# Kernel tuning notes

Measured on AMD Instinct MI355X. Metric: run time of the kernel, lower is better.

Reference implementation:

```python
import jax, jax.numpy as jnp
import numpy as np

N_HEADS = 32
N_KV = 8
HEAD_DIM = 128
THETA = 1000000.0


def setup_inputs() -> dict:
    key = jax.random.key(0)
    ks = jax.random.split(key, 7)
    batch, q_len, history = 4, 1024, 1024
    T = batch * q_len
    H = N_HEADS * HEAD_DIM  # 4096
    kv_len = q_len + history
    block_size = 64
    num_blocks = batch * (kv_len // block_size)  # 128
    s = 0.02
    return {
        'hidden_states': jax.random.normal(ks[0], (T, H), jnp.float32),
        'wq': jax.random.normal(ks[1], (H, N_HEADS * HEAD_DIM), jnp.float32) * s,
        'wk': jax.random.normal(ks[2], (H, N_KV * HEAD_DIM), jnp.float32) * s,
        'wv': jax.random.normal(ks[3], (H, N_KV * HEAD_DIM), jnp.float32) * s,
        'wo': jax.random.normal(ks[4], (N_HEADS * HEAD_DIM, H), jnp.float32) * s,
        'k_cache': jax.random.normal(ks[5], (num_blocks, block_size, N_KV, HEAD_DIM), jnp.float32),
        'v_cache': jax.random.normal(ks[6], (num_blocks, block_size, N_KV, HEAD_DIM), jnp.float32),
        'q_len': q_len,
        'history': history,
        'window': 1024,
    }


def _rotate_half(x):
    d = x.shape[-1]
    return jnp.concatenate([-x[..., d // 2:], x[..., :d // 2]], axis=-1)


def reference(hidden_states, wq, wk, wv, wo, k_cache, v_cache, q_len, history, window):
    T, H = hidden_states.shape
    batch = T // q_len
    kv_len = q_len + history
    nb, bs, n_kv, d = k_cache.shape
    blocks_per_seq = kv_len // bs
    # block table: sequence b owns contiguous blocks (paged layout)
    block_offsets = jnp.arange(batch * blocks_per_seq).reshape(batch, blocks_per_seq)

    # QKV projections
    q = (hidden_states @ wq).reshape(T, N_HEADS, d)
    k = (hidden_states @ wk).reshape(T, n_kv, d)
    v = (hidden_states @ wv).reshape(T, n_kv, d)

    # RoPE using 1d position ids (global positions of new tokens)
    pos = jnp.broadcast_to(history + jnp.arange(q_len), (batch, q_len)).reshape(T)
    inv_freq = 1.0 / (THETA ** (jnp.arange(0, d, 2, dtype=jnp.float32) / d))
    freqs = pos[:, None].astype(jnp.float32) * inv_freq[None, :]
    emb = jnp.concatenate([freqs, freqs], axis=-1)  # [T, d]
    cos = jnp.cos(emb)[:, None, :].astype(q.dtype)
    sin = jnp.sin(emb)[:, None, :].astype(q.dtype)
    q = q * cos + _rotate_half(q) * sin
    k = k * cos + _rotate_half(k) * sin

    # fill_kv_cache: scatter new K/V into paged slots history..kv_len-1
    new_pos = history + jnp.arange(q_len)  # [q_len]
    slot = (block_offsets[:, new_pos // bs] * bs + new_pos % bs).reshape(T)
    k_flat = k_cache.reshape(nb * bs, n_kv, d).at[slot].set(k)
    v_flat = v_cache.reshape(nb * bs, n_kv, d).at[slot].set(v)

    # paged gather of the full KV window per sequence
    all_pos = jnp.arange(kv_len)
    gslot = block_offsets[:, all_pos // bs] * bs + all_pos % bs  # [batch, kv_len]
    k_all = k_flat[gslot]  # [batch, kv_len, n_kv, d]
    v_all = v_flat[gslot]

    # GQA: expand kv heads
    rep = N_HEADS // n_kv
    k_all = jnp.repeat(k_all, rep, axis=2)
    v_all = jnp.repeat(v_all, rep, axis=2)

    qb = q.reshape(batch, q_len, N_HEADS, d)
    scores = jnp.einsum('bqhd,bkhd->bhqk', qb, k_all) / jnp.sqrt(jnp.asarray(d, qb.dtype))

    # causal + sliding-window mask on global positions
    qpos = history + jnp.arange(q_len)
    kpos = jnp.arange(kv_len)
    mask = kpos[None, :] <= qpos[:, None]
    if window > 0:
        mask = mask & ((qpos[:, None] - kpos[None, :]) < window)
    neg = jnp.finfo(scores.dtype).min
    scores = jnp.where(mask[None, None], scores, neg)
    attn = jax.nn.softmax(scores, axis=-1)
    out = jnp.einsum('bhqk,bkhd->bqhd', attn, v_all).reshape(T, N_HEADS * d)
    return out @ wo
```

## Files before the change

### kernel.cpp

```cpp
#include <hip/hip_runtime.h>
#include <hip/hip_bf16.h>

typedef __bf16 bf16x8 __attribute__((ext_vector_type(8)));
typedef __bf16 bf16x4 __attribute__((ext_vector_type(4)));
typedef float  f32x4  __attribute__((ext_vector_type(4)));

#define QL 1024
#define NH 32
#define NKV 8
#define HD 128
#define KVLEN 2048
#define QKV_LD 6144

typedef const __attribute__((address_space(1))) void gv_t;
typedef __attribute__((address_space(3))) void lv_t;
__device__ __forceinline__ void gll16(const void* g, void* l) {
  __builtin_amdgcn_global_load_lds((gv_t*)g, (lv_t*)l, 16, 0, 0);
}

__global__ __launch_bounds__(256) void cast_plain(const float* __restrict__ in,
                                                  __bf16* __restrict__ out, int n4) {
  int i = blockIdx.x * 256 + threadIdx.x;
  if (i >= n4) return;
  float4 v = ((const float4*)in)[i];
  bf16x4 o;
  o[0] = (__bf16)v.x; o[1] = (__bf16)v.y; o[2] = (__bf16)v.z; o[3] = (__bf16)v.w;
  ((bf16x4*)out)[i] = o;
}

__global__ __launch_bounds__(256) void transpose_cast(const float* __restrict__ in,
                                                      __bf16* __restrict__ out,
                                                      int R, int C) {
  __shared__ __bf16 tile[64][65];
  int r0 = blockIdx.y * 64, c0 = blockIdx.x * 64;
  int t = threadIdx.x;
  int tr = t >> 4, tc = (t & 15) * 4;
#pragma unroll
  for (int pass = 0; pass < 4; pass++) {
    int r = pass * 16 + tr;
    float4 v = *(const float4*)(in + (size_t)(r0 + r) * C + c0 + tc);
    tile[r][tc + 0] = (__bf16)v.x;
    tile[r][tc + 1] = (__bf16)v.y;
    tile[r][tc + 2] = (__bf16)v.z;
    tile[r][tc + 3] = (__bf16)v.w;
  }
  __syncthreads();
#pragma unroll
  for (int pass = 0; pass < 4; pass++) {
    int cc = pass * 16 + tr;
    bf16x4 o;
#pragma unroll
    for (int j = 0; j < 4; j++) o[j] = tile[tc + j][cc];
    *(bf16x4*)(out + (size_t)(c0 + cc) * R + r0 + tc) = o;
  }
}

template <int OUT_BF16>
__global__ __launch_bounds__(256) void gemm_bt(const __bf16* __restrict__ A,
                                               const __bf16* __restrict__ Bt,
                                               void* __restrict__ Cout,
                                               int M, int N, int K) {
  __shared__ __attribute__((aligned(16))) __bf16 sA[128 * 32];
  __shared__ __attribute__((aligned(16))) __bf16 sB[128 * 32];
  const int tid = threadIdx.x;
  const int lane = tid & 63;
  const int wave = tid >> 6;
  const int wm = wave >> 1, wn = wave & 1;
  const int quad = lane >> 4, l16 = lane & 15;
  const int row0 = blockIdx.y * 128, col0 = blockIdx.x * 128;

  const int rloc = tid >> 2;
  const int qsel = (tid & 3) ^ ((tid >> 3) & 3);
  const __bf16* gA0 = A + (size_t)(row0 + rloc) * K + qsel * 8;
  const __bf16* gA1 = A + (size_t)(row0 + 64 + rloc) * K + qsel * 8;
  const __bf16* gB0 = Bt + (size_t)(col0 + rloc) * K + qsel * 8;
  const __bf16* gB1 = Bt + (size_t)(col0 + 64 + rloc) * K + qsel * 8;
  __bf16* lA0 = sA + tid * 8;
  __bf16* lA1 = sA + 2048 + tid * 8;
  __bf16* lB0 = sB + tid * 8;
  __bf16* lB1 = sB + 2048 + tid * 8;

  const int xsw = (l16 >> 1) & 3;

  f32x4 acc[4][4];
#pragma unroll
  for (int mt = 0; mt < 4; mt++)
#pragma unroll
    for (int nt = 0; nt < 4; nt++) acc[mt][nt] = (f32x4){0.f, 0.f, 0.f, 0.f};

  for (int k0 = 0; k0 < K; k0 += 32) {
    __syncthreads();
    gll16(gA0 + k0, lA0);
    gll16(gA1 + k0, lA1);
    gll16(gB0 + k0, lB0);
    gll16(gB1 + k0, lB1);
    __syncthreads();
    bf16x8 af[4], bfr[4];
#pragma unroll
    for (int mt = 0; mt < 4; mt++)
      af[mt] = *(const bf16x8*)(sA + (wm * 64 + mt * 16 + l16) * 32 + (quad ^ xsw) * 8);
#pragma unroll
    for (int nt = 0; nt < 4; nt++)
      bfr[nt] = *(const bf16x8*)(sB + (wn * 64 + nt * 16 + l16) * 32 + (quad ^ xsw) * 8);
#pragma unroll
    for (int mt = 0; mt < 4; mt++)
#pragma unroll
      for (int nt = 0; nt < 4; nt++)
        acc[mt][nt] = __builtin_amdgcn_mfma_f32_16x16x32_bf16(af[mt], bfr[nt],
                                                              acc[mt][nt], 0, 0, 0);
  }

#pragma unroll
  for (int mt = 0; mt < 4; mt++) {
#pragma unroll
    for (int r = 0; r < 4; r++) {
      int grow = row0 + wm * 64 + mt * 16 + quad * 4 + r;
#pragma unroll
      for (int nt = 0; nt < 4; nt++) {
        int gcol = col0 + wn * 64 + nt * 16 + l16;
        float v = acc[mt][nt][r];
        if (OUT_BF16)
          ((__bf16*)Cout)[(size_t)grow * N + gcol] = (__bf16)v;
        else
          ((float*)Cout)[(size_t)grow * N + gcol] = v;
      }
    }
  }
}

__global__ __launch_bounds__(256) void rope_kernel(__bf16* __restrict__ qkv) {
  int idx = blockIdx.x * 256 + threadIdx.x;
  int m = idx & 63;
  int rest = idx >> 6;
  int t = rest / 40;
  int head = rest - t * 40;
  int i = t & (QL - 1);
  float pos = (float)(1024 + i);
  float ang = pos * exp2f(-(float)m * 0.31143075889569403f);
  float c = cosf(ang), sn = sinf(ang);
  size_t base = (size_t)t * QKV_LD + head * HD;
  float x0 = (float)qkv[base + m];
  float x1 = (float)qkv[base + 64 + m];
  qkv[base + m]      = (__bf16)(x0 * c - x1 * sn);
  qkv[base + 64 + m] = (__bf16)(x1 * c + x0 * sn);
}

__global__ __launch_bounds__(256) void kv_build_k(const float* __restrict__ kcache,
                                                  const __bf16* __restrict__ qkv,
                                                  __bf16* __restrict__ k_all) {
  int idx = blockIdx.x * 256 + threadIdx.x;
  int d8 = (idx & 15) * 8;
  int p = (idx >> 4) & (KVLEN - 1);
  int bk = idx >> 15;
  int b = bk >> 3, kvh = bk & 7;
  __bf16* dst = k_all + ((size_t)bk * KVLEN + p) * HD + d8;
  if (p < 1024) {
    const float* src = kcache + ((size_t)(b * KVLEN + p) * NKV + kvh) * HD + d8;
    bf16x8 o;
#pragma unroll
    for (int j = 0; j < 8; j++) o[j] = (__bf16)src[j];
    *(bf16x8*)dst = o;
  } else {
    const __bf16* src = qkv + (size_t)(b * QL + p - 1024) * QKV_LD + 4096 + kvh * HD + d8;
    *(bf16x8*)dst = *(const bf16x8*)src;
  }
}

__global__ __launch_bounds__(256) void kv_build_vT(const float* __restrict__ vcache,
                                                   const __bf16* __restrict__ qkv,
                                                   __bf16* __restrict__ v_allT) {
  __shared__ __bf16 tile[64][130];
  int blk = blockIdx.x;
  int pt = blk & 31, bk = blk >> 5;
  int b = bk >> 3, kvh = bk & 7;
  int p0 = pt * 64;
  int t = threadIdx.x;
  int lr = t >> 4, d8 = (t & 15) * 8;
#pragma unroll
  for (int pass = 0; pass < 4; pass++) {
    int pl = pass * 16 + lr;
    int p = p0 + pl;
    if (p < 1024) {
      const float* src = vcache + ((size_t)(b * KVLEN + p) * NKV + kvh) * HD + d8;
#pragma unroll
      for (int j = 0; j < 8; j++) tile[pl][d8 + j] = (__bf16)src[j];
    } else {
      const __bf16* src = qkv + (size_t)(b * QL + p - 1024) * QKV_LD + 5120 + kvh * HD + d8;
      bf16x8 v = *(const bf16x8*)src;
#pragma unroll
      for (int j = 0; j < 8; j++) tile[pl][d8 + j] = v[j];
    }
  }
  __syncthreads();
#pragma unroll
  for (int pass = 0; pass < 4; pass++) {
    int d = (t >> 3) + pass * 32;
    int ps = (t & 7) * 8;
    bf16x8 o;
#pragma unroll
    for (int j = 0; j < 8; j++) o[j] = tile[ps + j][d];
    *(bf16x8*)(v_allT + ((size_t)bk * HD + d) * KVLEN + p0 + ps) = o;
  }
}

__global__ __launch_bounds__(256) void attn_kernel(const __bf16* __restrict__ qkv,
                                                   const __bf16* __restrict__ k_all,
                                                   const __bf16* __restrict__ v_allT,
                                                   __bf16* __restrict__ out) {
  __shared__ __attribute__((aligned(16))) __bf16 sK[64 * 128];
  __shared__ __attribute__((aligned(16))) __bf16 sV[128 * 64];
  __shared__ __attribute__((aligned(16))) __bf16 sP[4][32 * 72];
  const int tid = threadIdx.x;
  const int lane = tid & 63;
  const int wave = tid >> 6;
  const int quad = lane >> 4, l16 = lane & 15;
  const int bid = blockIdx.x;
  const int b = bid & 3;
  const int kvh = (bid >> 2) & 7;
  const int qt = bid >> 5;
  const int h = kvh * 4 + wave;
  const int i0 = qt * 32;

  const __bf16* kb = k_all + (size_t)(b * NKV + kvh) * KVLEN * HD;
  const __bf16* vb = v_allT + (size_t)(b * NKV + kvh) * HD * KVLEN;

  bf16x8 qf[2][4];
#pragma unroll
  for (int mt = 0; mt < 2; mt++) {
    const __bf16* qb = qkv + (size_t)(b * QL + i0 + mt * 16 + l16) * QKV_LD + h * HD + quad * 8;
#pragma unroll
    for (int kc = 0; kc < 4; kc++) qf[mt][kc] = *(const bf16x8*)(qb + kc * 32);
  }

  int kgo[4], vgo[4];
#pragma unroll
  for (int j = 0; j < 4; j++) {
    int g = wave * 4 + j;
    kgo[j] = (g * 4 + quad) * HD + (l16 ^ (g & 7)) * 8;
    int d = g * 8 + (lane >> 3);
    vgo[j] = d * KVLEN + ((lane & 7) ^ ((lane >> 3) & 7)) * 8;
  }
  __bf16* kls = sK + (wave * 4) * 512 + lane * 8;
  __bf16* vls = sV + (wave * 4) * 512 + lane * 8;

  f32x4 o[8][2];
#pragma unroll
  for (int dt = 0; dt < 8; dt++)
#pragma unroll
    for (int mt = 0; mt < 2; mt++) o[dt][mt] = (f32x4){0.f, 0.f, 0.f, 0.f};
  f32x4 lac[2];
  lac[0] = (f32x4){0.f, 0.f, 0.f, 0.f};
  lac[1] = (f32x4){0.f, 0.f, 0.f, 0.f};

  bf16x8 ones;
#pragma unroll
  for (int j = 0; j < 8; j++) ones[j] = (__bf16)1.0f;

  __bf16* myP = &sP[wave][0];
  const float ES = 0.12751744f;

  const int cs = (i0 + 1) & ~63;
  const int xsw = l16 & 7;

#pragma unroll
  for (int j = 0; j < 4; j++) gll16(kb + (size_t)cs * HD + kgo[j], kls + j * 512);
#pragma unroll
  for (int j = 0; j < 4; j++) gll16(vb + (size_t)cs + vgo[j], vls + j * 512);

  for (int ci = 0; ci < 17; ci++) {
    const int c = cs + ci * 64;
    __syncthreads();
    f32x4 s[2][4];
#pragma unroll
    for (int nt = 0; nt < 4; nt++) {
      s[0][nt] = (f32x4){0.f, 0.f, 0.f, 0.f};
      s[1][nt] = (f32x4){0.f, 0.f, 0.f, 0.f};
      const __bf16* kp = sK + (4 * l16 + nt) * HD;
#pragma unroll
      for (int kc = 0; kc < 4; kc++) {
        bf16x8 kf = *(const bf16x8*)(kp + ((4 * kc + quad) ^ xsw) * 8);
        s[0][nt] = __builtin_amdgcn_mfma_f32_16x16x32_bf16(qf[0][kc], kf, s[0][nt], 0, 0, 0);
        s[1][nt] = __builtin_amdgcn_mfma_f32_16x16x32_bf16(qf[1][kc], kf, s[1][nt], 0, 0, 0);
      }
    }
    __syncthreads();
    if (ci < 16) {
#pragma unroll
      for (int j = 0; j < 4; j++) gll16(kb + (size_t)(c + 64) * HD + kgo[j], kls + j * 512);
    }
    const bool full = (c >= i0 + 32) && (c <= i0 + 961);
#pragma unroll
    for (int mt = 0; mt < 2; mt++) {
#pragma unroll
      for (int r = 0; r < 4; r++) {
        bf16x4 pk;
        if (full) {
#pragma unroll
          for (int nt = 0; nt < 4; nt++) pk[nt] = (__bf16)exp2f(s[mt][nt][r] * ES);
        } else {
          const int irow = i0 + mt * 16 + quad * 4 + r;
#pragma unroll
          for (int nt = 0; nt < 4; nt++) {
            const int kk = c + 4 * l16 + nt;
            const bool valid = (kk > irow) && (kk <= irow + 1024);
            pk[nt] = valid ? (__bf16)exp2f(s[mt][nt][r] * ES) : (__bf16)0.0f;
          }
        }
        *(bf16x4*)(myP + (mt * 16 + quad * 4 + r) * 72 + 4 * l16) = pk;
      }
    }
    asm volatile("s_waitcnt lgkmcnt(0)" ::: "memory");
#pragma unroll
    for (int kc = 0; kc < 2; kc++) {
      bf16x8 pf0 = *(const bf16x8*)(myP + (l16) * 72 + kc * 32 + quad * 8);
      bf16x8 pf1 = *(const bf16x8*)(myP + (16 + l16) * 72 + kc * 32 + quad * 8);
      lac[0] = __builtin_amdgcn_mfma_f32_16x16x32_bf16(pf0, ones, lac[0], 0, 0, 0);
      lac[1] = __builtin_amdgcn_mfma_f32_16x16x32_bf16(pf1, ones, lac[1], 0, 0, 0);
#pragma unroll
      for (int dt = 0; dt < 8; dt++) {
        bf16x8 vf = *(const bf16x8*)(sV + (dt * 16 + l16) * 64 + ((kc * 4 + quad) ^ xsw) * 8);
        o[dt][0] = __builtin_amdgcn_mfma_f32_16x16x32_bf16(pf0, vf, o[dt][0], 0, 0, 0);
        o[dt][1] = __builtin_amdgcn_mfma_f32_16x16x32_bf16(pf1, vf, o[dt][1], 0, 0, 0);
      }
    }
    __syncthreads();
    if (ci < 16) {
#pragma unroll
      for (int j = 0; j < 4; j++) gll16(vb + (size_t)(c + 64) + vgo[j], vls + j * 512);
    }
  }

  float inv[2][4];
#pragma unroll
  for (int mt = 0; mt < 2; mt++)
#pragma unroll
    for (int r = 0; r < 4; r++) inv[mt][r] = 1.0f / lac[mt][r];
#pragma unroll
  for (int dt = 0; dt < 8; dt++)
#pragma unroll
    for (int mt = 0; mt < 2; mt++)
#pragma unroll
      for (int r = 0; r < 4; r++)
        out[(size_t)(b * QL + i0 + mt * 16 + quad * 4 + r) * (NH * HD) + h * HD + dt * 16 + l16] =
            (__bf16)(o[dt][mt][r] * inv[mt][r]);
}

extern "C" void kernel_launch(void* const* d_in, const int* in_sizes, int n_in,
                              void* d_out, int out_size, void* d_ws, size_t ws_size,
                              hipStream_t stream) {
  const float* hidden = (const float*)d_in[0];
  const float* wq = (const float*)d_in[1];
  const float* wk = (const float*)d_in[2];
  const float* wv = (const float*)d_in[3];
  const float* wo = (const float*)d_in[4];
  const float* kcache = (const float*)d_in[5];
  const float* vcache = (const float*)d_in[6];
  (void)in_sizes; (void)n_in; (void)out_size; (void)ws_size;

  char* w = (char*)d_ws;
  __bf16* hid_b  = (__bf16*)(w);
  __bf16* wqkvT  = (__bf16*)(w + 33554432ULL);
  __bf16* qkv    = (__bf16*)(w + 83886080ULL);
  __bf16* k_all  = (__bf16*)(w + 134217728ULL);
  __bf16* v_allT = (__bf16*)(w + 150994944ULL);
  __bf16* attn   = hid_b;
  __bf16* woT    = wqkvT;

  cast_plain<<<16384, 256, 0, stream>>>(hidden, hid_b, 4194304);
  transpose_cast<<<dim3(64, 64), 256, 0, stream>>>(wq, wqkvT, 4096, 4096);
  transpose_cast<<<dim3(16, 64), 256, 0, stream>>>(wk, wqkvT + 16777216ULL, 4096, 1024);
  transpose_cast<<<dim3(16, 64), 256, 0, stream>>>(wv, wqkvT + 20971520ULL, 4096, 1024);
  gemm_bt<1><<<dim3(48, 32), 256, 0, stream>>>(hid_b, wqkvT, (void*)qkv, 4096, 6144, 4096);
  rope_kernel<<<40960, 256, 0, stream>>>(qkv);
  kv_build_k<<<4096, 256, 0, stream>>>(kcache, qkv, k_all);
  kv_build_vT<<<1024, 256, 0, stream>>>(vcache, qkv, v_allT);
  attn_kernel<<<1024, 256, 0, stream>>>(qkv, k_all, v_allT, attn);
  transpose_cast<<<dim3(64, 64), 256, 0, stream>>>(wo, woT, 4096, 4096);
  gemm_bt<0><<<dim3(32, 32), 256, 0, stream>>>(attn, woT, d_out, 4096, 4096, 4096);
}
```

Measured before the change: 830.3 us.

## Replace GEMM with 256x256-tile, 4-stage pipelined, XCD-swizzled kernel

Swaps the 128x128 single-buffered GEMM for a 256x256-tile kernel with 512 threads, a 4-deep LDS ring fed by asynchronous global-to-LDS loads, split half-tile MFMA phases with s_setprio, and a grid swizzle that spreads adjacent tiles across XCDs. It targets the load/compute serialization and barrier stalls of the old loop, and raises data reuse per tile. In exchange it uses 128KB of LDS and many more accumulator registers. Grid size shrinks to 384/256 blocks, which may underfill 256 CUs with a tail.

Result: faster. 773.9 us (-6.8%).

```diff
diff --git a/kernel.cpp b/kernel.cpp
--- a/kernel.cpp
+++ b/kernel.cpp
@@ -56,68 +56,116 @@
 }
 
 template <int OUT_BF16>
-__global__ __launch_bounds__(256) void gemm_bt(const __bf16* __restrict__ A,
-                                               const __bf16* __restrict__ Bt,
-                                               void* __restrict__ Cout,
-                                               int M, int N, int K) {
-  __shared__ __attribute__((aligned(16))) __bf16 sA[128 * 32];
-  __shared__ __attribute__((aligned(16))) __bf16 sB[128 * 32];
+__global__ __launch_bounds__(512, 2) void gemm256(const __bf16* __restrict__ A,
+                                                  const __bf16* __restrict__ Bt,
+                                                  void* __restrict__ Cout,
+                                                  int M, int N, int K) {
+  __shared__ __attribute__((aligned(16))) __bf16 sA[4][8192];
+  __shared__ __attribute__((aligned(16))) __bf16 sB[4][8192];
   const int tid = threadIdx.x;
   const int lane = tid & 63;
   const int wave = tid >> 6;
-  const int wm = wave >> 1, wn = wave & 1;
+  const int wm = wave >> 2, wn = wave & 3;
   const int quad = lane >> 4, l16 = lane & 15;
-  const int row0 = blockIdx.y * 128, col0 = blockIdx.x * 128;
-
-  const int rloc = tid >> 2;
+
+  const int nwg = gridDim.x;
+  const int id = blockIdx.x;
+  const int swz = (id & 7) * (nwg >> 3) + (id >> 3);
+  const int gx = N >> 8;
+  const int by = swz / gx, bx = swz - by * gx;
+  const int row0 = by * 256, col0 = bx * 256;
+
   const int qsel = (tid & 3) ^ ((tid >> 3) & 3);
-  const __bf16* gA0 = A + (size_t)(row0 + rloc) * K + qsel * 8;
-  const __bf16* gA1 = A + (size_t)(row0 + 64 + rloc) * K + qsel * 8;
-  const __bf16* gB0 = Bt + (size_t)(col0 + rloc) * K + qsel * 8;
-  const __bf16* gB1 = Bt + (size_t)(col0 + 64 + rloc) * K + qsel * 8;
-  __bf16* lA0 = sA + tid * 8;
-  __bf16* lA1 = sA + 2048 + tid * 8;
-  __bf16* lB0 = sB + tid * 8;
-  __bf16* lB1 = sB + 2048 + tid * 8;
+  const __bf16* pA0 = A + (size_t)(row0 + (tid >> 2)) * K + qsel * 8;
+  const __bf16* pA1 = pA0 + (size_t)128 * K;
+  const __bf16* pB0 = Bt + (size_t)(col0 + (tid >> 2)) * K + qsel * 8;
+  const __bf16* pB1 = pB0 + (size_t)128 * K;
 
   const int xsw = (l16 >> 1) & 3;
-
-  f32x4 acc[4][4];
-#pragma unroll
-  for (int mt = 0; mt < 4; mt++)
+  const int aoff = (wm * 128 + l16) * 32 + (quad ^ xsw) * 8;
+  const int boff = (wn * 64 + l16) * 32 + (quad ^ xsw) * 8;
+
+  f32x4 acc[8][4];
+#pragma unroll
+  for (int mt = 0; mt < 8; mt++)
 #pragma unroll
     for (int nt = 0; nt < 4; nt++) acc[mt][nt] = (f32x4){0.f, 0.f, 0.f, 0.f};
 
-  for (int k0 = 0; k0 < K; k0 += 32) {
-    __syncthreads();
-    gll16(gA0 + k0, lA0);
-    gll16(gA1 + k0, lA1);
-    gll16(gB0 + k0, lB0);
-    gll16(gB1 + k0, lB1);
-    __syncthreads();
-    bf16x8 af[4], bfr[4];
-#pragma unroll
-    for (int mt = 0; mt < 4; mt++)
-      af[mt] = *(const bf16x8*)(sA + (wm * 64 + mt * 16 + l16) * 32 + (quad ^ xsw) * 8);
-#pragma unroll
-    for (int nt = 0; nt < 4; nt++)
-      bfr[nt] = *(const bf16x8*)(sB + (wn * 64 + nt * 16 + l16) * 32 + (quad ^ xsw) * 8);
-#pragma unroll
-    for (int mt = 0; mt < 4; mt++)
-#pragma unroll
-      for (int nt = 0; nt < 4; nt++)
-        acc[mt][nt] = __builtin_amdgcn_mfma_f32_16x16x32_bf16(af[mt], bfr[nt],
-                                                              acc[mt][nt], 0, 0, 0);
-  }
-
-#pragma unroll
-  for (int mt = 0; mt < 4; mt++) {
-#pragma unroll
-    for (int r = 0; r < 4; r++) {
-      int grow = row0 + wm * 64 + mt * 16 + quad * 4 + r;
-#pragma unroll
-      for (int nt = 0; nt < 4; nt++) {
-        int gcol = col0 + wn * 64 + nt * 16 + l16;
+  const int nT = K >> 5;
+
+  for (int pt = 0; pt < 3; ++pt) {
+    __bf16* dA = &sA[pt][0];
+    __bf16* dB = &sB[pt][0];
+    gll16(pA0, dA + tid * 8);
+    gll16(pA1, dA + 4096 + tid * 8);
+    gll16(pB0, dB + tid * 8);
+    gll16(pB1, dB + 4096 + tid * 8);
+    pA0 += 32; pA1 += 32; pB0 += 32; pB1 += 32;
+  }
+  asm volatile("s_waitcnt vmcnt(8)" ::: "memory");
+  __builtin_amdgcn_s_barrier();
+
+  for (int t = 0; t < nT; ++t) {
+    const int bt = t & 3;
+    const bool st = (t + 3 < nT);
+    const __bf16* Ab = &sA[bt][aoff];
+    const __bf16* Bb = &sB[bt][boff];
+    __bf16* dA = &sA[(t + 3) & 3][0];
+    __bf16* dB = &sB[(t + 3) & 3][0];
+    bf16x8 a[4], b[4];
+
+#pragma unroll
+    for (int i = 0; i < 4; ++i) a[i] = *(const bf16x8*)(Ab + i * 512);
+#pragma unroll
+    for (int i = 0; i < 4; ++i) b[i] = *(const bf16x8*)(Bb + i * 512);
+    if (st) {
+      gll16(pA0, dA + tid * 8);
+      gll16(pA1, dA + 4096 + tid * 8);
+    }
+    asm volatile("" ::: "memory");
+    __builtin_amdgcn_s_barrier();
+    __builtin_amdgcn_s_setprio(1);
+#pragma unroll
+    for (int mt = 0; mt < 4; ++mt)
+#pragma unroll
+      for (int nt = 0; nt < 4; ++nt)
+        acc[mt][nt] = __builtin_amdgcn_mfma_f32_16x16x32_bf16(a[mt], b[nt], acc[mt][nt], 0, 0, 0);
+    __builtin_amdgcn_s_setprio(0);
+    __builtin_amdgcn_s_barrier();
+
+#pragma unroll
+    for (int i = 0; i < 4; ++i) a[i] = *(const bf16x8*)(Ab + (4 + i) * 512);
+    if (st) {
+      gll16(pB0, dB + tid * 8);
+      gll16(pB1, dB + 4096 + tid * 8);
+      pA0 += 32; pA1 += 32; pB0 += 32; pB1 += 32;
+    }
+    if (t + 3 < nT) {
+      asm volatile("s_waitcnt vmcnt(8)" ::: "memory");
+    } else if (t + 2 < nT) {
+      asm volatile("s_waitcnt vmcnt(4)" ::: "memory");
+    } else if (t + 1 < nT) {
+      asm volatile("s_waitcnt vmcnt(0)" ::: "memory");
+    }
+    __builtin_amdgcn_s_barrier();
+    __builtin_amdgcn_s_setprio(1);
+#pragma unroll
+    for (int mt = 0; mt < 4; ++mt)
+#pragma unroll
+      for (int nt = 0; nt < 4; ++nt)
+        acc[4 + mt][nt] = __builtin_amdgcn_mfma_f32_16x16x32_bf16(a[mt], b[nt], acc[4 + mt][nt], 0, 0, 0);
+    __builtin_amdgcn_s_setprio(0);
+    __builtin_amdgcn_s_barrier();
+  }
+
+#pragma unroll
+  for (int mt = 0; mt < 8; ++mt) {
+#pragma unroll
+    for (int r = 0; r < 4; ++r) {
+      const int grow = row0 + wm * 128 + mt * 16 + quad * 4 + r;
+#pragma unroll
+      for (int nt = 0; nt < 4; ++nt) {
+        const int gcol = col0 + wn * 64 + nt * 16 + l16;
         float v = acc[mt][nt][r];
         if (OUT_BF16)
           ((__bf16*)Cout)[(size_t)grow * N + gcol] = (__bf16)v;
@@ -370,11 +418,11 @@
   transpose_cast<<<dim3(64, 64), 256, 0, stream>>>(wq, wqkvT, 4096, 4096);
   transpose_cast<<<dim3(16, 64), 256, 0, stream>>>(wk, wqkvT + 16777216ULL, 4096, 1024);
   transpose_cast<<<dim3(16, 64), 256, 0, stream>>>(wv, wqkvT + 20971520ULL, 4096, 1024);
-  gemm_bt<1><<<dim3(48, 32), 256, 0, stream>>>(hid_b, wqkvT, (void*)qkv, 4096, 6144, 4096);
+  gemm256<1><<<dim3(384), 512, 0, stream>>>(hid_b, wqkvT, (void*)qkv, 4096, 6144, 4096);
   rope_kernel<<<40960, 256, 0, stream>>>(qkv);
   kv_build_k<<<4096, 256, 0, stream>>>(kcache, qkv, k_all);
   kv_build_vT<<<1024, 256, 0, stream>>>(vcache, qkv, v_allT);
   attn_kernel<<<1024, 256, 0, stream>>>(qkv, k_all, v_allT, attn);
   transpose_cast<<<dim3(64, 64), 256, 0, stream>>>(wo, woT, 4096, 4096);
-  gemm_bt<0><<<dim3(32, 32), 256, 0, stream>>>(attn, woT, d_out, 4096, 4096, 4096);
-}
+  gemm256<0><<<dim3(256), 512, 0, stream>>>(attn, woT, d_out, 4096, 4096, 4096);
+}
```
